# Performance work log

Hardware: AMD Instinct MI355X
Metric: run time of the kernel (lower is better)

## Reference

```python
import jax, jax.numpy as jnp
import numpy as np

N_HEAD = 12
HEAD_DIM = 64
EPS = 1e-6
ROPE_BASE = 10000.0


def rms_norm(x, w):
    x32 = x.astype(jnp.float32)
    var = jnp.mean(x32 * x32, axis=-1, keepdims=True)
    xn = x32 * jax.lax.rsqrt(var + EPS)
    return w * xn.astype(x.dtype)


def rotate_half(x):
    x1, x2 = jnp.split(x, 2, axis=-1)
    return jnp.concatenate((-x2, x1), axis=-1)


def rope_cos_sin(seq_len, dtype):
    inv_freq = 1.0 / (ROPE_BASE ** (jnp.arange(0, HEAD_DIM, 2, dtype=jnp.float32) / HEAD_DIM))
    pos = jnp.arange(seq_len, dtype=jnp.float32)
    freqs = pos[:, None] * inv_freq[None, :]          # [S, HEAD_DIM//2]
    emb = jnp.concatenate((freqs, freqs), axis=-1)    # [S, HEAD_DIM]
    # shape [1, 1, S, HEAD_DIM] (batch, head, seq, dim) after unsqueeze_dim=1
    return emb[None, None].astype(dtype), None  # placeholder, see below


def setup_inputs() -> dict:
    key = jax.random.key(0)
    ks = jax.random.split(key, 9)
    B, S, D, F = 1, 4096, 768, 2048
    s = 0.02
    return {
        "hidden_states": jax.random.normal(ks[0], (B, S, D), jnp.float32),
        "w_q": jax.random.normal(ks[1], (D, D), jnp.float32) * s,
        "w_k": jax.random.normal(ks[2], (D, D), jnp.float32) * s,
        "w_v": jax.random.normal(ks[3], (D, D), jnp.float32) * s,
        "w_o": jax.random.normal(ks[4], (D, D), jnp.float32) * s,
        "w_gate": jax.random.normal(ks[5], (D, F), jnp.float32) * s,
        "w_up": jax.random.normal(ks[6], (D, F), jnp.float32) * s,
        "w_down": jax.random.normal(ks[7], (F, D), jnp.float32) * s,
        "w_norm1": jnp.ones((D,), jnp.float32),
        "w_norm2": jnp.ones((D,), jnp.float32),
    }


def attention(x, w_q, w_k, w_v, w_o):
    B, S, D = x.shape
    scale = HEAD_DIM ** -0.5
    # project and split heads: [B, H, S, hd]
    q = (x @ w_q).reshape(B, S, N_HEAD, HEAD_DIM).transpose(0, 2, 1, 3)
    k = (x @ w_k).reshape(B, S, N_HEAD, HEAD_DIM).transpose(0, 2, 1, 3)
    v = (x @ w_v).reshape(B, S, N_HEAD, HEAD_DIM).transpose(0, 2, 1, 3)
    # rotary embedding (position_ids = arange(S))
    inv_freq = 1.0 / (ROPE_BASE ** (jnp.arange(0, HEAD_DIM, 2, dtype=jnp.float32) / HEAD_DIM))
    pos = jnp.arange(S, dtype=jnp.float32)
    freqs = pos[:, None] * inv_freq[None, :]
    emb = jnp.concatenate((freqs, freqs), axis=-1)          # [S, hd]
    cos = jnp.cos(emb).astype(x.dtype)[None, None]          # [1,1,S,hd]
    sin = jnp.sin(emb).astype(x.dtype)[None, None]
    q = q * cos + rotate_half(q) * sin
    k = k * cos + rotate_half(k) * sin
    # eager attention with causal mask (materialized, as in the original)
    scores = jnp.einsum("bhqd,bhkd->bhqk", q, k) * scale
    causal = jnp.triu(jnp.ones((S, S), dtype=bool), k=1)
    scores = jnp.where(causal, jnp.finfo(scores.dtype).min, scores)
    attn = jax.nn.softmax(scores.astype(jnp.float32), axis=-1).astype(q.dtype)
    out = jnp.einsum("bhqk,bhkd->bhqd", attn, v)
    out = out.transpose(0, 2, 1, 3).reshape(B, S, D)
    return out @ w_o


def reference(hidden_states, w_q, w_k, w_v, w_o, w_gate, w_up, w_down, w_norm1, w_norm2):
    x = hidden_states
    h = x + attention(rms_norm(x, w_norm1), w_q, w_k, w_v, w_o)
    y = rms_norm(h, w_norm2)
    ffn = (jax.nn.silu(y @ w_gate) * (y @ w_up)) @ w_down
    return h + ffn
```

## Files before the change

### kernel.cpp

```cpp
#include <hip/hip_runtime.h>
#include <hip/hip_bf16.h>

typedef __attribute__((ext_vector_type(8))) short s8v;
typedef __attribute__((ext_vector_type(4))) float f4v;
typedef __attribute__((ext_vector_type(16))) float f16v;
typedef __attribute__((ext_vector_type(4))) unsigned u4v;

typedef __attribute__((address_space(1))) const void as1_void;
typedef __attribute__((address_space(3))) void as3_void;

__device__ __forceinline__ void gl16(const void* g, void* l) {
  __builtin_amdgcn_global_load_lds((as1_void*)g, (as3_void*)l, 16, 0, 0);
}

__device__ __forceinline__ float b2f(int u) {
  union { float f; unsigned i; } c; c.i = ((unsigned)(u & 0xFFFF)) << 16; return c.f;
}
__device__ __forceinline__ unsigned short f2b(float f) {
  union { float f; unsigned i; } c; c.f = f;
  unsigned r = c.i + 0x7FFFu + ((c.i >> 16) & 1u);
  return (unsigned short)(r >> 16);
}
__device__ __forceinline__ unsigned pk2(float lo, float hi) {
  unsigned u;
  asm("v_cvt_pk_bf16_f32 %0, %1, %2" : "=v"(u) : "v"(lo), "v"(hi));
  return u;
}

#define MFMA16(a, b, c) __builtin_amdgcn_mfma_f32_16x16x32_bf16((a), (b), (c), 0, 0, 0)
#define MFMA32(a, b, c) __builtin_amdgcn_mfma_f32_32x32x16_bf16((a), (b), (c), 0, 0, 0)

struct Seg { const float* src; unsigned short* dst; int K; int N; int nbn; int nblocks; int mode; };
struct PrepArgs { Seg seg[8]; float* ct; float* st; };

__global__ __launch_bounds__(256) void prep_k(PrepArgs a) {
  int b = blockIdx.x, si = 0;
  while (si < 7 && b >= a.seg[si].nblocks) { b -= a.seg[si].nblocks; ++si; }
  const Seg s = a.seg[si];
  const int tid = threadIdx.x;
  if (s.mode == 3) {
    const int t = b * 256 + tid;
    const int sq = t >> 5, d = t & 31;
    const float inv = powf(10000.0f, -(float)d * (1.0f / 32.0f));
    const float ang = (float)sq * inv;
    a.ct[t] = cosf(ang);
    a.st[t] = sinf(ang);
    return;
  }
  __shared__ float tile[32][33];
  const int tx = tid & 31, ty = tid >> 5;
  const int bn = b % s.nbn, bk = b / s.nbn;
#pragma unroll
  for (int i = 0; i < 32; i += 8)
    tile[ty + i][tx] = s.src[(size_t)(bk * 32 + ty + i) * s.N + bn * 32 + tx];
  __syncthreads();
#pragma unroll
  for (int i = 0; i < 32; i += 8) {
    int row;
    if (s.mode == 0)      row = bn * 32 + ty + i;
    else                  row = bn * 64 + (s.mode == 2 ? 32 : 0) + ty + i;
    s.dst[(size_t)row * s.K + bk * 32 + tx] = f2b(tile[tx][ty + i]);
  }
}

__global__ __launch_bounds__(256) void rmsnorm_k(const float* __restrict__ x,
    const float* __restrict__ w, unsigned short* __restrict__ out) {
  const int row = blockIdx.x, tid = threadIdx.x;
  const float* xr = x + (size_t)row * 768;
  float v0 = xr[tid], v1 = xr[tid + 256], v2 = xr[tid + 512];
  float ss = v0 * v0 + v1 * v1 + v2 * v2;
#pragma unroll
  for (int m = 1; m < 64; m <<= 1) ss += __shfl_xor(ss, m, 64);
  __shared__ float sred[4];
  if ((tid & 63) == 0) sred[tid >> 6] = ss;
  __syncthreads();
  const float tot = sred[0] + sred[1] + sred[2] + sred[3];
  const float rn = rsqrtf(tot * (1.0f / 768.0f) + 1e-6f);
  unsigned short* orow = out + (size_t)row * 768;
  orow[tid]       = f2b(v0 * rn * w[tid]);
  orow[tid + 256] = f2b(v1 * rn * w[tid + 256]);
  orow[tid + 512] = f2b(v2 * rn * w[tid + 512]);
}

template <int EPI, int BN>
__global__ __launch_bounds__(256) void gemm_bt(const unsigned short* __restrict__ A,
    const unsigned short* __restrict__ Bt, unsigned short* __restrict__ Cb,
    float* __restrict__ Cf, const float* __restrict__ R, int K, int ldc,
    const float* __restrict__ ct, const float* __restrict__ st) {
  constexpr int ABYTES = 128 * 32 * 2;
  constexpr int BBYTES = BN * 32 * 2;
  constexpr int MR = (BN == 128) ? 4 : 2;
  __shared__ unsigned short As[3 * 128 * 32];
  __shared__ unsigned short Bs[3 * BN * 32];
  const int tid = threadIdx.x;
  const int lane = tid & 63, wid = tid >> 6;
  const int wrow = (BN == 128) ? (wid >> 1) * 64 : wid * 32;
  const int wcol = (BN == 128) ? (wid & 1) * 64 : 0;
  const int l15 = lane & 15, l4 = lane >> 4;
  const int bm = blockIdx.y, bn = blockIdx.x;

  f4v acc[MR][4] = {};

  const int o0 = tid * 16, o1 = tid * 16 + 4096;
  const int r0 = o0 >> 6, c0 = o0 & 63;
  const int r1 = o1 >> 6, c1 = o1 & 63;
  const size_t ldab = (size_t)K * 2;
  const char* Abyte = (const char*)A;
  const char* Bbyte = (const char*)Bt;
  const size_t a0 = (size_t)(bm * 128 + r0) * ldab + c0;
  const size_t a1 = (size_t)(bm * 128 + r1) * ldab + c1;
  const size_t b0 = (size_t)(bn * BN + r0) * ldab + c0;
  const size_t b1 = (size_t)(bn * BN + r1) * ldab + c1;
  char* AsB = (char*)As;
  char* BsB = (char*)Bs;
  const int uoff = wid << 10;

#define STAGEK(I, SL) do { const size_t kb = (size_t)(I) * 64;                 \
    char* Aw = AsB + (SL) * ABYTES;                                            \
    char* Bw = BsB + (SL) * BBYTES;                                            \
    gl16(Abyte + a0 + kb, Aw + uoff);                                          \
    gl16(Abyte + a1 + kb, Aw + uoff + 4096);                                   \
    gl16(Bbyte + b0 + kb, Bw + uoff);                                          \
    if constexpr (BN == 128) gl16(Bbyte + b1 + kb, Bw + uoff + 4096); } while (0)

  const int NI = K >> 5;
  STAGEK(0, 0);
  STAGEK(1, 1);
  int sel = 0, nsl = 2;

  for (int i = 0; i < NI; ++i) {
    if (i < NI - 1) {
      if constexpr (BN == 128) asm volatile("s_waitcnt vmcnt(4)" ::: "memory");
      else                     asm volatile("s_waitcnt vmcnt(3)" ::: "memory");
    } else {
      asm volatile("s_waitcnt vmcnt(0)" ::: "memory");
    }
    __builtin_amdgcn_s_barrier();
    __builtin_amdgcn_sched_barrier(0);
    if (i + 2 < NI) STAGEK(i + 2, nsl);
    const char* Ar = AsB + sel * ABYTES;
    const char* Br = BsB + sel * BBYTES;
    s8v af[MR], bf[4];
#pragma unroll
    for (int m = 0; m < MR; ++m)
      af[m] = *(const s8v*)(Ar + (wrow + m * 16 + l15) * 64 + l4 * 16);
#pragma unroll
    for (int n = 0; n < 4; ++n)
      bf[n] = *(const s8v*)(Br + (wcol + n * 16 + l15) * 64 + l4 * 16);
    __builtin_amdgcn_s_setprio(1);
#pragma unroll
    for (int m = 0; m < MR; ++m)
#pragma unroll
      for (int n = 0; n < 4; ++n) acc[m][n] = MFMA16(af[m], bf[n], acc[m][n]);
    __builtin_amdgcn_s_setprio(0);
    sel = (sel == 2) ? 0 : sel + 1;
    nsl = (nsl == 2) ? 0 : nsl + 1;
  }
#undef STAGEK

  const int row0 = bm * 128 + wrow;
  const int col0 = bn * BN + wcol;

  if (EPI == 2 && bn < 12) {
#pragma unroll
    for (int m = 0; m < MR; ++m)
#pragma unroll
      for (int r = 0; r < 4; ++r) {
        const int row = row0 + m * 16 + l4 * 4 + r;
#pragma unroll
        for (int n = 0; n < 2; ++n) {
          const int d = n * 16 + l15;
          const float c  = ct[row * 32 + d];
          const float sn = st[row * 32 + d];
          const float aa = acc[m][n][r], bb = acc[m][n + 2][r];
          acc[m][n][r]     = aa * c - bb * sn;
          acc[m][n + 2][r] = bb * c + aa * sn;
        }
      }
  }

  if (EPI == 3) {
    const int wcx = wcol >> 6;
    const int colb = (bn * 2 + wcx) * 32;
#pragma unroll
    for (int m = 0; m < MR; ++m)
#pragma unroll
      for (int n = 0; n < 2; ++n)
#pragma unroll
        for (int r = 0; r < 4; ++r) {
          const int row = row0 + m * 16 + l4 * 4 + r;
          const float g = acc[m][n][r], u = acc[m][n + 2][r];
          const float val = g * u / (1.0f + __expf(-g));
          Cb[(size_t)row * 2048 + colb + n * 16 + l15] = f2b(val);
        }
    return;
  }

#pragma unroll
  for (int m = 0; m < MR; ++m)
#pragma unroll
    for (int n = 0; n < 4; ++n)
#pragma unroll
      for (int r = 0; r < 4; ++r) {
        const int row = row0 + m * 16 + l4 * 4 + r;
        const int col = col0 + n * 16 + l15;
        const float v = acc[m][n][r];
        if (EPI == 1) {
          Cf[(size_t)row * ldc + col] = v + R[(size_t)row * ldc + col];
        } else {
          Cb[(size_t)row * ldc + col] = f2b(v);
        }
      }
}

__global__ __launch_bounds__(256, 3) void flash_k(const unsigned short* __restrict__ qkv,
    float4* __restrict__ Opart, float2* __restrict__ ml) {
  const int kh = blockIdx.x, p = blockIdx.y, h = blockIdx.z;
  const int qbA = 63 - p;
  const int tid = threadIdx.x;
  const int wv = tid >> 6, lane = tid & 63;
  const int l31 = lane & 31, h8 = lane >> 5;
  const int myqb = (wv & 1) ? p : qbA;
  const int qrel = (wv >> 1) * 32 + l31;
  const int q_abs = myqb * 64 + qrel;

  __shared__ unsigned short Ks[2][64 * 72];
  __shared__ unsigned short Vt[2][64 * 72];

  const unsigned short* qp = qkv + h * 64;
  const unsigned short* kp = qkv + 768 + h * 64;
  const unsigned short* vp = qkv + 1536 + h * 64;

  s8v qf[4];
#pragma unroll
  for (int c = 0; c < 4; ++c)
    qf[c] = *(const s8v*)(qp + (size_t)q_abs * 2304 + c * 16 + h8 * 8);

  f16v o0 = {}, o1 = {};
  float m_s = -1e30f, l_s = 0.f;

  const int krow = tid >> 3, kc = (tid & 7) * 8;
  const int vj = tid & 31, vd0 = (tid >> 5) * 8;

  s8v ka, kb, va, vb;
#define LOADT(T) do { const size_t k0n = (size_t)(T) * 64;                    \
    ka = *(const s8v*)(kp + (k0n + krow) * 2304 + kc);                        \
    kb = *(const s8v*)(kp + (k0n + krow + 32) * 2304 + kc);                   \
    va = *(const s8v*)(vp + (k0n + 2 * vj) * 2304 + vd0);                     \
    vb = *(const s8v*)(vp + (k0n + 2 * vj + 1) * 2304 + vd0); } while (0)
#define WRITET(BUF) do {                                                      \
    *(s8v*)(Ks[BUF] + krow * 72 + kc) = ka;                                   \
    *(s8v*)(Ks[BUF] + (krow + 32) * 72 + kc) = kb;                            \
    unsigned* vtw = (unsigned*)(Vt[BUF] + (size_t)vd0 * 72 + 2 * vj);         \
    _Pragma("unroll")                                                         \
    for (int i = 0; i < 8; ++i)                                               \
      vtw[i * 36] = ((unsigned)(unsigned short)va[i]) |                       \
                    (((unsigned)(unsigned short)vb[i]) << 16); } while (0)

  LOADT(kh);
  WRITET(0);
  if (kh + 2 <= qbA) LOADT(kh + 2);
  __syncthreads();

  for (int t = kh; t <= qbA; t += 2) {
    const int cur = (t >> 1) & 1;
    if (t <= myqb) {
      f16v s0 = {}, s1 = {};
      __builtin_amdgcn_s_setprio(1);
#pragma unroll
      for (int c = 0; c < 4; ++c) {
        const s8v kf0 = *(const s8v*)(Ks[cur] + l31 * 72 + c * 16 + h8 * 8);
        const s8v kf1 = *(const s8v*)(Ks[cur] + (32 + l31) * 72 + c * 16 + h8 * 8);
        s0 = MFMA32(kf0, qf[c], s0);
        s1 = MFMA32(kf1, qf[c], s1);
      }
      __builtin_amdgcn_s_setprio(0);
#pragma unroll
      for (int r = 0; r < 16; ++r) { s0[r] *= 0.125f; s1[r] *= 0.125f; }
      if (t == myqb) {
#pragma unroll
        for (int r = 0; r < 16; ++r) {
          const int koff = (r & 3) + 8 * (r >> 2) + 4 * h8;
          if (koff > qrel) s0[r] = -1e30f;
          if (koff + 32 > qrel) s1[r] = -1e30f;
        }
      }
      float red[8];
#pragma unroll
      for (int i = 0; i < 8; ++i)
        red[i] = fmaxf(fmaxf(s0[i], s0[i + 8]), fmaxf(s1[i], s1[i + 8]));
#pragma unroll
      for (int i = 0; i < 4; ++i) red[i] = fmaxf(red[i], red[i + 4]);
      float mloc = fmaxf(fmaxf(red[0], red[1]), fmaxf(red[2], red[3]));
      mloc = fmaxf(mloc, __shfl_xor(mloc, 32));
      if (__any(mloc > m_s + 8.f)) {
        const float mn = fmaxf(m_s, mloc);
        const float corr = __expf(m_s - mn);
        m_s = mn; l_s *= corr;
#pragma unroll
        for (int r = 0; r < 16; ++r) { o0[r] *= corr; o1[r] *= corr; }
      }
#pragma unroll
      for (int r = 0; r < 16; ++r) {
        s0[r] = __expf(s0[r] - m_s);
        s1[r] = __expf(s1[r] - m_s);
      }
      float sm[8];
#pragma unroll
      for (int i = 0; i < 8; ++i) sm[i] = (s0[i] + s0[i + 8]) + (s1[i] + s1[i + 8]);
#pragma unroll
      for (int i = 0; i < 4; ++i) sm[i] += sm[i + 4];
      float ps = (sm[0] + sm[1]) + (sm[2] + sm[3]);
      ps += __shfl_xor(ps, 32);
      l_s += ps;

      unsigned pk0[8], pk1[8];
#pragma unroll
      for (int g = 0; g < 4; ++g)
#pragma unroll
        for (int j = 0; j < 2; ++j) {
          pk0[g * 2 + j] = pk2(s0[g * 4 + 2 * j], s0[g * 4 + 2 * j + 1]);
          pk1[g * 2 + j] = pk2(s1[g * 4 + 2 * j], s1[g * 4 + 2 * j + 1]);
        }
      __builtin_amdgcn_s_setprio(1);
#pragma unroll
      for (int c = 0; c < 4; ++c) {
        const int g0 = (c & 1) * 2, g1 = g0 + 1;
        const unsigned pA0 = (c & 2) ? pk1[g0 * 2 + 0] : pk0[g0 * 2 + 0];
        const unsigned pA1 = (c & 2) ? pk1[g0 * 2 + 1] : pk0[g0 * 2 + 1];
        const unsigned pB0 = (c & 2) ? pk1[g1 * 2 + 0] : pk0[g1 * 2 + 0];
        const unsigned pB1 = (c & 2) ? pk1[g1 * 2 + 1] : pk0[g1 * 2 + 1];
        const unsigned t00 = __shfl_xor((int)pA0, 32);
        const unsigned t01 = __shfl_xor((int)pA1, 32);
        const unsigned t10 = __shfl_xor((int)pB0, 32);
        const unsigned t11 = __shfl_xor((int)pB1, 32);
        union { u4v u; s8v s; } pf;
        pf.u[0] = h8 ? t10 : pA0;
        pf.u[1] = h8 ? t11 : pA1;
        pf.u[2] = h8 ? pB0 : t00;
        pf.u[3] = h8 ? pB1 : t01;
        const s8v vf0 = *(const s8v*)(Vt[cur] + l31 * 72 + c * 16 + h8 * 8);
        const s8v vf1 = *(const s8v*)(Vt[cur] + (32 + l31) * 72 + c * 16 + h8 * 8);
        o0 = MFMA32(vf0, pf.s, o0);
        o1 = MFMA32(vf1, pf.s, o1);
      }
      __builtin_amdgcn_s_setprio(0);
    }
    if (t + 2 <= qbA) {
      WRITET(cur ^ 1);
      if (t + 4 <= qbA) LOADT(t + 4);
      __syncthreads();
    }
  }

  const size_t obase = (size_t)kh * 12 * 16 * 4096;
#pragma unroll
  for (int g = 0; g < 4; ++g) {
    const float4 v0 = make_float4(o0[g * 4], o0[g * 4 + 1], o0[g * 4 + 2], o0[g * 4 + 3]);
    const float4 v1 = make_float4(o1[g * 4], o1[g * 4 + 1], o1[g * 4 + 2], o1[g * 4 + 3]);
    const int dg0 = 2 * g + h8;
    const int dg1 = 8 + 2 * g + h8;
    Opart[obase + ((size_t)h * 16 + dg0) * 4096 + q_abs] = v0;
    Opart[obase + ((size_t)h * 16 + dg1) * 4096 + q_abs] = v1;
  }
  if (h8 == 0)
    ml[(size_t)kh * 12 * 4096 + (size_t)h * 4096 + q_abs] = make_float2(m_s, l_s);
#undef LOADT
#undef WRITET
}

__global__ __launch_bounds__(256) void combine_k(const float4* __restrict__ Opart,
    const float2* __restrict__ ml, unsigned short* __restrict__ out) {
  const int u = blockIdx.x * 256 + threadIdx.x;
  const int q = u & 4095;
  const int rest = u >> 12;
  const int dgrp = rest & 15;
  const int h = rest >> 4;
  const float2 e0 = ml[h * 4096 + q];
  const float2 e1 = ml[12 * 4096 + h * 4096 + q];
  const float mx = fmaxf(e0.x, e1.x);
  const float w0 = __expf(e0.x - mx), w1 = __expf(e1.x - mx);
  const float inv = 1.0f / (w0 * e0.y + w1 * e1.y);
  const size_t idx = ((size_t)h * 16 + dgrp) * 4096 + q;
  const float4 a = Opart[idx];
  const float4 b = Opart[(size_t)12 * 16 * 4096 + idx];
  const int dbase = (dgrp < 8) ? 4 * dgrp : 32 + 4 * (dgrp - 8);
  ushort4 r;
  r.x = f2b((w0 * a.x + w1 * b.x) * inv);
  r.y = f2b((w0 * a.y + w1 * b.y) * inv);
  r.z = f2b((w0 * a.z + w1 * b.z) * inv);
  r.w = f2b((w0 * a.w + w1 * b.w) * inv);
  *(ushort4*)(out + (size_t)q * 768 + h * 64 + dbase) = r;
}

extern "C" void kernel_launch(void* const* d_in, const int* in_sizes, int n_in,
                              void* d_out, int out_size, void* d_ws, size_t ws_size,
                              hipStream_t stream) {
  const float* x    = (const float*)d_in[0];
  const float* w_q  = (const float*)d_in[1];
  const float* w_k  = (const float*)d_in[2];
  const float* w_v  = (const float*)d_in[3];
  const float* w_o  = (const float*)d_in[4];
  const float* w_g  = (const float*)d_in[5];
  const float* w_u  = (const float*)d_in[6];
  const float* w_d  = (const float*)d_in[7];
  const float* w_n1 = (const float*)d_in[8];
  const float* w_n2 = (const float*)d_in[9];
  (void)in_sizes; (void)n_in; (void)out_size; (void)ws_size;

  char* ws = (char*)d_ws;
  size_t off = 0;
  auto alloc = [&](size_t bytes) { char* p = ws + off; off += (bytes + 255) & ~(size_t)255; return p; };
  unsigned short* wqkvT = (unsigned short*)alloc(2304ull * 768 * 2);
  unsigned short* woT   = (unsigned short*)alloc(768ull * 768 * 2);
  unsigned short* wguT  = (unsigned short*)alloc(4096ull * 768 * 2);
  unsigned short* wdT   = (unsigned short*)alloc(768ull * 2048 * 2);
  float* ct             = (float*)alloc(4096ull * 32 * 4);
  float* st             = (float*)alloc(4096ull * 32 * 4);
  unsigned short* xn    = (unsigned short*)alloc(4096ull * 768 * 2);
  unsigned short* qkv   = (unsigned short*)alloc(4096ull * 2304 * 2);
  unsigned short* attn  = (unsigned short*)alloc(4096ull * 768 * 2);
  float* hbuf           = (float*)alloc(4096ull * 768 * 4);
  unsigned short* ybuf  = (unsigned short*)alloc(4096ull * 768 * 2);
  unsigned short* ffn   = (unsigned short*)alloc(4096ull * 2048 * 2);
  float4* Opart         = (float4*)alloc(2ull * 12 * 16 * 4096 * 16);
  float2* mlb           = (float2*)alloc(2ull * 12 * 4096 * 8);

  PrepArgs pa;
  pa.seg[0] = { w_q, wqkvT,                 768,  768, 24,  576, 0 };
  pa.seg[1] = { w_k, wqkvT + 768 * 768,     768,  768, 24,  576, 0 };
  pa.seg[2] = { w_v, wqkvT + 2 * 768 * 768, 768,  768, 24,  576, 0 };
  pa.seg[3] = { w_o, woT,                   768,  768, 24,  576, 0 };
  pa.seg[4] = { w_g, wguT,                  768, 2048, 64, 1536, 1 };
  pa.seg[5] = { w_u, wguT,                  768, 2048, 64, 1536, 2 };
  pa.seg[6] = { w_d, wdT,                  2048,  768, 24, 1536, 0 };
  pa.seg[7] = { nullptr, nullptr, 0, 0, 0, 512, 3 };
  pa.ct = ct; pa.st = st;
  const int prep_blocks = 576 * 4 + 1536 * 3 + 512;

  prep_k<<<prep_blocks, 256, 0, stream>>>(pa);
  rmsnorm_k<<<4096, 256, 0, stream>>>(x, w_n1, xn);
  gemm_bt<2, 128><<<dim3(18, 32), 256, 0, stream>>>(xn, wqkvT, qkv, nullptr, nullptr, 768, 2304, ct, st);
  flash_k<<<dim3(2, 32, 12), 256, 0, stream>>>(qkv, Opart, mlb);
  combine_k<<<3072, 256, 0, stream>>>(Opart, mlb, attn);
  gemm_bt<1, 64><<<dim3(12, 32), 256, 0, stream>>>(attn, woT, nullptr, hbuf, x, 768, 768, nullptr, nullptr);
  rmsnorm_k<<<4096, 256, 0, stream>>>(hbuf, w_n2, ybuf);
  gemm_bt<3, 128><<<dim3(32, 32), 256, 0, stream>>>(ybuf, wguT, ffn, nullptr, nullptr, 768, 2048, nullptr, nullptr);
  gemm_bt<1, 64><<<dim3(12, 32), 256, 0, stream>>>(ffn, wdT, nullptr, (float*)d_out, hbuf, 2048, 768, nullptr, nullptr);
}
```

Measured before the change: 225.4 us.

## Merge split-K flash halves into one 512-thread block with in-LDS combine

The two key-split halves of the attention kernel, previously separate blocks that wrote fp32 partials to global memory for a separate combine kernel, now run as two 256-thread halves of one 512-thread block. The halves merge their partial outputs through shared memory and write bf16 results directly, which removes the combine launch and the partial-buffer traffic. The softmax scale and log2(e) are folded into Q in the QKV GEMM epilogue so the kernel can use exp2, and v_max3 is used for the row-max reduction. The cost is a doubled LDS footprint, a 512-thread launch bound that may limit occupancy, and a __syncthreads on every iteration.

```diff
diff --git a/kernel.cpp b/kernel.cpp
--- a/kernel.cpp
+++ b/kernel.cpp
@@ -25,6 +25,11 @@
   unsigned u;
   asm("v_cvt_pk_bf16_f32 %0, %1, %2" : "=v"(u) : "v"(lo), "v"(hi));
   return u;
+}
+__device__ __forceinline__ float max3f(float a, float b, float c) {
+  float d;
+  asm("v_max3_f32 %0, %1, %2, %3" : "=v"(d) : "v"(a), "v"(b), "v"(c));
+  return d;
 }
 
 #define MFMA16(a, b, c) __builtin_amdgcn_mfma_f32_16x16x32_bf16((a), (b), (c), 0, 0, 0)
@@ -178,6 +183,15 @@
         }
       }
   }
+  if (EPI == 2 && bn < 6) {
+    const float QSC = 0.18033688011112042f;
+#pragma unroll
+    for (int m = 0; m < MR; ++m)
+#pragma unroll
+      for (int n = 0; n < 4; ++n)
+#pragma unroll
+        for (int r = 0; r < 4; ++r) acc[m][n][r] *= QSC;
+  }
 
   if (EPI == 3) {
     const int wcx = wcol >> 6;
@@ -213,19 +227,23 @@
       }
 }
 
-__global__ __launch_bounds__(256, 3) void flash_k(const unsigned short* __restrict__ qkv,
-    float4* __restrict__ Opart, float2* __restrict__ ml) {
-  const int kh = blockIdx.x, p = blockIdx.y, h = blockIdx.z;
-  const int qbA = 63 - p;
+__global__ __launch_bounds__(512, 4) void flash_k(const unsigned short* __restrict__ qkv,
+    unsigned short* __restrict__ out) {
+  const int p = blockIdx.x, h = blockIdx.y;
+  const int qbA = 63 - p, qbB = p;
   const int tid = threadIdx.x;
   const int wv = tid >> 6, lane = tid & 63;
   const int l31 = lane & 31, h8 = lane >> 5;
-  const int myqb = (wv & 1) ? p : qbA;
-  const int qrel = (wv >> 1) * 32 + l31;
+  const int h4 = wv >> 2, idx = wv & 3;
+  const bool roleL = ((idx & 1) == h4);
+  const int rowhalf = idx >> 1;
+  const int myqb = roleL ? qbA : qbB;
+  const int qrel = rowhalf * 32 + l31;
   const int q_abs = myqb * 64 + qrel;
 
-  __shared__ unsigned short Ks[2][64 * 72];
-  __shared__ unsigned short Vt[2][64 * 72];
+  __shared__ char smem[73728];
+#define KSB(hf, bf) ((unsigned short*)(smem + ((((hf) * 2 + (bf)) * 2 + 0) * 9216)))
+#define VTB(hf, bf) ((unsigned short*)(smem + ((((hf) * 2 + (bf)) * 2 + 1) * 9216)))
 
   const unsigned short* qp = qkv + h * 64;
   const unsigned short* kp = qkv + 768 + h * 64;
@@ -239,8 +257,9 @@
   f16v o0 = {}, o1 = {};
   float m_s = -1e30f, l_s = 0.f;
 
-  const int krow = tid >> 3, kc = (tid & 7) * 8;
-  const int vj = tid & 31, vd0 = (tid >> 5) * 8;
+  const int tid2 = tid & 255;
+  const int krow = tid2 >> 3, kc = (tid2 & 7) * 8;
+  const int vj = tid2 & 31, vd0 = (tid2 >> 5) * 8;
 
   s8v ka, kb, va, vb;
 #define LOADT(T) do { const size_t k0n = (size_t)(T) * 64;                    \
@@ -249,34 +268,37 @@
     va = *(const s8v*)(vp + (k0n + 2 * vj) * 2304 + vd0);                     \
     vb = *(const s8v*)(vp + (k0n + 2 * vj + 1) * 2304 + vd0); } while (0)
 #define WRITET(BUF) do {                                                      \
-    *(s8v*)(Ks[BUF] + krow * 72 + kc) = ka;                                   \
-    *(s8v*)(Ks[BUF] + (krow + 32) * 72 + kc) = kb;                            \
-    unsigned* vtw = (unsigned*)(Vt[BUF] + (size_t)vd0 * 72 + 2 * vj);         \
+    unsigned short* ksw = KSB(h4, BUF);                                       \
+    *(s8v*)(ksw + krow * 72 + kc) = ka;                                       \
+    *(s8v*)(ksw + (krow + 32) * 72 + kc) = kb;                                \
+    unsigned* vtw = (unsigned*)(VTB(h4, BUF) + (size_t)vd0 * 72 + 2 * vj);    \
     _Pragma("unroll")                                                         \
     for (int i = 0; i < 8; ++i)                                               \
       vtw[i * 36] = ((unsigned)(unsigned short)va[i]) |                       \
                     (((unsigned)(unsigned short)vb[i]) << 16); } while (0)
 
-  LOADT(kh);
+  LOADT(h4);
   WRITET(0);
-  if (kh + 2 <= qbA) LOADT(kh + 2);
+  if (h4 + 2 <= qbA) LOADT(h4 + 2);
   __syncthreads();
 
-  for (int t = kh; t <= qbA; t += 2) {
-    const int cur = (t >> 1) & 1;
+  const int NT = (qbA >> 1) + 1;
+  for (int tt = 0; tt < NT; ++tt) {
+    const int t = 2 * tt + h4;
+    const int cur = tt & 1;
     if (t <= myqb) {
+      const unsigned short* Ksr = KSB(h4, cur);
+      const unsigned short* Vtr = VTB(h4, cur);
       f16v s0 = {}, s1 = {};
       __builtin_amdgcn_s_setprio(1);
 #pragma unroll
       for (int c = 0; c < 4; ++c) {
-        const s8v kf0 = *(const s8v*)(Ks[cur] + l31 * 72 + c * 16 + h8 * 8);
-        const s8v kf1 = *(const s8v*)(Ks[cur] + (32 + l31) * 72 + c * 16 + h8 * 8);
+        const s8v kf0 = *(const s8v*)(Ksr + l31 * 72 + c * 16 + h8 * 8);
+        const s8v kf1 = *(const s8v*)(Ksr + (32 + l31) * 72 + c * 16 + h8 * 8);
         s0 = MFMA32(kf0, qf[c], s0);
         s1 = MFMA32(kf1, qf[c], s1);
       }
       __builtin_amdgcn_s_setprio(0);
-#pragma unroll
-      for (int r = 0; r < 16; ++r) { s0[r] *= 0.125f; s1[r] *= 0.125f; }
       if (t == myqb) {
 #pragma unroll
         for (int r = 0; r < 16; ++r) {
@@ -285,25 +307,23 @@
           if (koff + 32 > qrel) s1[r] = -1e30f;
         }
       }
-      float red[8];
+      float u[8];
 #pragma unroll
       for (int i = 0; i < 8; ++i)
-        red[i] = fmaxf(fmaxf(s0[i], s0[i + 8]), fmaxf(s1[i], s1[i + 8]));
-#pragma unroll
-      for (int i = 0; i < 4; ++i) red[i] = fmaxf(red[i], red[i + 4]);
-      float mloc = fmaxf(fmaxf(red[0], red[1]), fmaxf(red[2], red[3]));
+        u[i] = fmaxf(max3f(s0[i], s0[i + 8], s1[i]), s1[i + 8]);
+      float mloc = fmaxf(max3f(max3f(max3f(u[0], u[1], u[2]), u[3], u[4]), u[5], u[6]), u[7]);
       mloc = fmaxf(mloc, __shfl_xor(mloc, 32));
-      if (__any(mloc > m_s + 8.f)) {
+      if (__any(mloc > m_s + 11.0f)) {
         const float mn = fmaxf(m_s, mloc);
-        const float corr = __expf(m_s - mn);
+        const float corr = exp2f(m_s - mn);
         m_s = mn; l_s *= corr;
 #pragma unroll
         for (int r = 0; r < 16; ++r) { o0[r] *= corr; o1[r] *= corr; }
       }
 #pragma unroll
       for (int r = 0; r < 16; ++r) {
-        s0[r] = __expf(s0[r] - m_s);
-        s1[r] = __expf(s1[r] - m_s);
+        s0[r] = exp2f(s0[r] - m_s);
+        s1[r] = exp2f(s1[r] - m_s);
       }
       float sm[8];
 #pragma unroll
@@ -339,8 +359,8 @@
         pf.u[1] = h8 ? t11 : pA1;
         pf.u[2] = h8 ? pB0 : t00;
         pf.u[3] = h8 ? pB1 : t01;
-        const s8v vf0 = *(const s8v*)(Vt[cur] + l31 * 72 + c * 16 + h8 * 8);
-        const s8v vf1 = *(const s8v*)(Vt[cur] + (32 + l31) * 72 + c * 16 + h8 * 8);
+        const s8v vf0 = *(const s8v*)(Vtr + l31 * 72 + c * 16 + h8 * 8);
+        const s8v vf1 = *(const s8v*)(Vtr + (32 + l31) * 72 + c * 16 + h8 * 8);
         o0 = MFMA32(vf0, pf.s, o0);
         o1 = MFMA32(vf1, pf.s, o1);
       }
@@ -349,48 +369,49 @@
     if (t + 2 <= qbA) {
       WRITET(cur ^ 1);
       if (t + 4 <= qbA) LOADT(t + 4);
-      __syncthreads();
     }
-  }
-
-  const size_t obase = (size_t)kh * 12 * 16 * 4096;
-#pragma unroll
-  for (int g = 0; g < 4; ++g) {
-    const float4 v0 = make_float4(o0[g * 4], o0[g * 4 + 1], o0[g * 4 + 2], o0[g * 4 + 3]);
-    const float4 v1 = make_float4(o1[g * 4], o1[g * 4 + 1], o1[g * 4 + 2], o1[g * 4 + 3]);
-    const int dg0 = 2 * g + h8;
-    const int dg1 = 8 + 2 * g + h8;
-    Opart[obase + ((size_t)h * 16 + dg0) * 4096 + q_abs] = v0;
-    Opart[obase + ((size_t)h * 16 + dg1) * 4096 + q_abs] = v1;
-  }
-  if (h8 == 0)
-    ml[(size_t)kh * 12 * 4096 + (size_t)h * 4096 + q_abs] = make_float2(m_s, l_s);
+    __syncthreads();
+  }
 #undef LOADT
 #undef WRITET
-}
-
-__global__ __launch_bounds__(256) void combine_k(const float4* __restrict__ Opart,
-    const float2* __restrict__ ml, unsigned short* __restrict__ out) {
-  const int u = blockIdx.x * 256 + threadIdx.x;
-  const int q = u & 4095;
-  const int rest = u >> 12;
-  const int dgrp = rest & 15;
-  const int h = rest >> 4;
-  const float2 e0 = ml[h * 4096 + q];
-  const float2 e1 = ml[12 * 4096 + h * 4096 + q];
-  const float mx = fmaxf(e0.x, e1.x);
-  const float w0 = __expf(e0.x - mx), w1 = __expf(e1.x - mx);
-  const float inv = 1.0f / (w0 * e0.y + w1 * e1.y);
-  const size_t idx = ((size_t)h * 16 + dgrp) * 4096 + q;
-  const float4 a = Opart[idx];
-  const float4 b = Opart[(size_t)12 * 16 * 4096 + idx];
-  const int dbase = (dgrp < 8) ? 4 * dgrp : 32 + 4 * (dgrp - 8);
-  ushort4 r;
-  r.x = f2b((w0 * a.x + w1 * b.x) * inv);
-  r.y = f2b((w0 * a.y + w1 * b.y) * inv);
-  r.z = f2b((w0 * a.z + w1 * b.z) * inv);
-  r.w = f2b((w0 * a.w + w1 * b.w) * inv);
-  *(ushort4*)(out + (size_t)q * 768 + h * 64 + dbase) = r;
+
+  float* fup = (float*)smem;
+  float* mup = (float*)(smem + 32768);
+  if (h4) {
+    const int base = (idx * 64 + lane) * 32;
+#pragma unroll
+    for (int r = 0; r < 16; ++r) { fup[base + r] = o0[r]; fup[base + 16 + r] = o1[r]; }
+    mup[(idx * 64 + lane) * 2]     = m_s;
+    mup[(idx * 64 + lane) * 2 + 1] = l_s;
+  }
+  __syncthreads();
+  unsigned short* obuf = (unsigned short*)(smem + 36864);
+  if (!h4) {
+    const int pb = ((idx ^ 1) * 64 + lane);
+    const float m2 = mup[pb * 2], l2 = mup[pb * 2 + 1];
+    const float mx = fmaxf(m_s, m2);
+    const float w0 = exp2f(m_s - mx), w1 = exp2f(m2 - mx);
+    const float inv = 1.0f / (w0 * l_s + w1 * l2);
+    const int Rr = (roleL ? 0 : 64) + qrel;
+    const int fb = pb * 32;
+#pragma unroll
+    for (int r = 0; r < 16; ++r) {
+      const int d0 = (r & 3) + 8 * (r >> 2) + 4 * h8;
+      obuf[Rr * 72 + d0]      = f2b((w0 * o0[r] + w1 * fup[fb + r]) * inv);
+      obuf[Rr * 72 + 32 + d0] = f2b((w0 * o1[r] + w1 * fup[fb + 16 + r]) * inv);
+    }
+  }
+  __syncthreads();
+  {
+    const int Rr = tid >> 2, ds = (tid & 3) * 16;
+    const int qb_o = (Rr < 64) ? qbA : qbB;
+    const int qr = Rr & 63;
+    unsigned short* dst = out + (size_t)(qb_o * 64 + qr) * 768 + h * 64 + ds;
+    *(s8v*)dst       = *(const s8v*)(obuf + Rr * 72 + ds);
+    *(s8v*)(dst + 8) = *(const s8v*)(obuf + Rr * 72 + ds + 8);
+  }
+#undef KSB
+#undef VTB
 }
 
 extern "C" void kernel_launch(void* const* d_in, const int* in_sizes, int n_in,
@@ -423,8 +444,6 @@
   float* hbuf           = (float*)alloc(4096ull * 768 * 4);
   unsigned short* ybuf  = (unsigned short*)alloc(4096ull * 768 * 2);
   unsigned short* ffn   = (unsigned short*)alloc(4096ull * 2048 * 2);
-  float4* Opart         = (float4*)alloc(2ull * 12 * 16 * 4096 * 16);
-  float2* mlb           = (float2*)alloc(2ull * 12 * 4096 * 8);
 
   PrepArgs pa;
   pa.seg[0] = { w_q, wqkvT,                 768,  768, 24,  576, 0 };
@@ -441,8 +460,7 @@
   prep_k<<<prep_blocks, 256, 0, stream>>>(pa);
   rmsnorm_k<<<4096, 256, 0, stream>>>(x, w_n1, xn);
   gemm_bt<2, 128><<<dim3(18, 32), 256, 0, stream>>>(xn, wqkvT, qkv, nullptr, nullptr, 768, 2304, ct, st);
-  flash_k<<<dim3(2, 32, 12), 256, 0, stream>>>(qkv, Opart, mlb);
-  combine_k<<<3072, 256, 0, stream>>>(Opart, mlb, attn);
+  flash_k<<<dim3(32, 12), 512, 0, stream>>>(qkv, attn);
   gemm_bt<1, 64><<<dim3(12, 32), 256, 0, stream>>>(attn, woT, nullptr, hbuf, x, 768, 768, nullptr, nullptr);
   rmsnorm_k<<<4096, 256, 0, stream>>>(hbuf, w_n2, ybuf);
   gemm_bt<3, 128><<<dim3(32, 32), 256, 0, stream>>>(ybuf, wguT, ffn, nullptr, nullptr, 768, 2048, nullptr, nullptr);
```

New measurement: 232.3 us. +3.1%, slower.
